# Optimization experiments

Hardware: AMD Instinct MI355X
Metric: run time of the kernel (lower is better)

The kernel has to match this reference:

```python
import jax, jax.numpy as jnp
import numpy as np

ALPHA = 1.0
M = K = N = 4096
VMAX = 16  # keep int32 accumulation far from overflow


def setup_inputs() -> dict:
    key = jax.random.key(0)
    k0, k1, k2 = jax.random.split(key, 3)
    input_tensor = jax.random.randint(k0, (M, N), 0, VMAX, dtype=jnp.int32)
    mat1 = jax.random.randint(k1, (M, K), 0, VMAX, dtype=jnp.int32)
    mat2 = jax.random.randint(k2, (K, N), 0, VMAX, dtype=jnp.int32)
    return {"input_tensor": input_tensor, "mat1": mat1, "mat2": mat2}


def reference(input_tensor, mat1, mat2):
    # int32 GEMM with int32 accumulation (matches torch int32 matmul)
    mm_int32 = jnp.matmul(mat1.astype(jnp.int32), mat2.astype(jnp.int32),
                          preferred_element_type=jnp.int32)
    sum_int32 = mm_int32 + input_tensor  # [M, N] int32
    return sum_int32.astype(jnp.float32) * jnp.float32(ALPHA)
```

## Files before the change

### kernel.cpp

```cpp
#include <hip/hip_runtime.h>

#define MK 4096
#define BK 128

typedef int v4i __attribute__((ext_vector_type(4)));
typedef int v16i __attribute__((ext_vector_type(16)));

#define MFMA32(a, b, c) __builtin_amdgcn_mfma_i32_32x32x32_i8(a, b, c, 0, 0, 0)

#define GLOAD_LDS16(gp, lp) \
  __builtin_amdgcn_global_load_lds((const __attribute__((address_space(1))) void*)(gp), \
                                   (__attribute__((address_space(3))) void*)(lp), 16, 0, 0)

#define SB() __builtin_amdgcn_sched_barrier(0)
#define BARRIER() __builtin_amdgcn_s_barrier()
#define WAIT_VM4() asm volatile("s_waitcnt vmcnt(4)" ::: "memory")
#define WAIT_VM0() asm volatile("s_waitcnt vmcnt(0)" ::: "memory")
#define NOWAIT() ((void)0)

__global__ __launch_bounds__(256) void cvt_kernel(const int* __restrict__ mat1,
                                                  char* __restrict__ A8,
                                                  const int* __restrict__ mat2,
                                                  char* __restrict__ B8T) {
  __shared__ char tile[64][68];
  if (blockIdx.x < 2048) {
    const int n4 = MK * MK / 4;
    int idx = blockIdx.x * 256 + threadIdx.x;
    const int stride = 2048 * 256;
    for (int i = idx; i < n4; i += stride) {
      int4 v = ((const int4*)mat1)[i];
      char4 c;
      c.x = (char)v.x; c.y = (char)v.y; c.z = (char)v.z; c.w = (char)v.w;
      ((char4*)A8)[i] = c;
    }
  } else {
    const int bid = blockIdx.x - 2048;
    const int t = threadIdx.x;
    const int n0 = (bid & 63) * 64, k0 = (bid >> 6) * 64;
#pragma unroll
    for (int r = 0; r < 16; ++r) {
      int k = k0 + r * 4 + (t >> 6);
      int n = n0 + (t & 63);
      tile[t & 63][r * 4 + (t >> 6)] = (char)mat2[(size_t)k * MK + n];
    }
    __syncthreads();
#pragma unroll
    for (int w = 0; w < 4; ++w) {
      int nl = w * 16 + (t >> 4);
      int kl = (t & 15) * 4;
      char4 c = *(const char4*)&tile[nl][kl];
      *(char4*)(B8T + (size_t)(n0 + nl) * MK + k0 + kl) = c;
    }
  }
}

__global__ __launch_bounds__(512, 2) void gemm_i8_kernel(const char* __restrict__ A8,
                                                         const char* __restrict__ B8T,
                                                         const int* __restrict__ inp,
                                                         float* __restrict__ out) {
  extern __shared__ char lds[];
  const int tid = threadIdx.x;
  const int wg = blockIdx.x;
  const int xcd = wg & 7, loc = wg >> 3;
  const int m0 = (((xcd >> 1) << 2) + (loc >> 3)) << 8;
  const int n0 = (((xcd & 1) << 3) + (loc & 7)) << 8;

  const int lane = tid & 63, wid = tid >> 6;
  const int wr = wid >> 2, wc = wid & 3;
  const int rl = lane & 31;
  const int khalf = lane >> 5;

  const int r15 = lane & 15;
  const int slotr = (lane >> 4) ^ ((r15 >> 1) & 3);
  const char* pAr = lds + wr * 8192 + r15 * 64 + slotr * 16;
  const char* pBr = lds + 65536 + wc * 4096 + r15 * 64 + slotr * 16;

  const int sblk = tid >> 7;
  const int skk = (tid >> 6) & 1;
  const int sr15 = (tid >> 2) & 15;
  const int sslot = tid & 3;
  const int sx = sslot ^ ((sr15 >> 1) & 3);
  const int srow = sblk * 32 + (sx & 1) * 16 + sr15;
  const int skb = skk * 32 + (sx >> 1) * 16;
  const char* pA = A8 + (size_t)(m0 + srow) * MK + skb;
  const char* pB = B8T + (size_t)(n0 + srow) * MK + skb;
  char* ldsw = lds + (tid & ~63) * 16;

#define STAGE_A_(NB_, H_, TN_) do {                                               \
    const char* s_ = pA + (TN_)*BK + (H_)*64;                                     \
    GLOAD_LDS16(s_,                    ldsw + ((NB_)*32768 + (H_)*16384));        \
    GLOAD_LDS16(s_ + (size_t)128 * MK, ldsw + ((NB_)*32768 + (H_)*16384 + 8192)); \
  } while (0)
#define STAGE_B_(NB_, H_, TN_) do {                                               \
    const char* s_ = pB + (TN_)*BK + (H_)*64;                                     \
    GLOAD_LDS16(s_,                    ldsw + (65536 + (NB_)*32768 + (H_)*16384)); \
    GLOAD_LDS16(s_ + (size_t)128 * MK, ldsw + (65536 + (NB_)*32768 + (H_)*16384 + 8192)); \
  } while (0)

#define AOFF(B_, KK_, MB_) ((B_)*32768 + ((KK_) >> 1) * 16384 + (MB_)*2048 + ((KK_)&1) * 1024)
#define BOFF(B_, KK_, NB_) ((B_)*32768 + ((KK_) >> 1) * 16384 + (NB_)*2048 + ((KK_)&1) * 1024)

#define REGION(B_, H_, TN_, DOST_, VMW_, DOSYNC_) do {                            \
    bf0 = *(const v4i*)(pBr + BOFF(B_, 2*(H_), 0));                               \
    af0 = *(const v4i*)(pAr + AOFF(B_, 2*(H_), 0));                               \
    af1 = *(const v4i*)(pAr + AOFF(B_, 2*(H_), 1));                               \
    af2 = *(const v4i*)(pAr + AOFF(B_, 2*(H_), 2));                               \
    af3 = *(const v4i*)(pAr + AOFF(B_, 2*(H_), 3));                               \
    bf1 = *(const v4i*)(pBr + BOFF(B_, 2*(H_), 1));                               \
    bg0 = *(const v4i*)(pBr + BOFF(B_, 2*(H_) + 1, 0));                           \
    ag0 = *(const v4i*)(pAr + AOFF(B_, 2*(H_) + 1, 0));                           \
    ag1 = *(const v4i*)(pAr + AOFF(B_, 2*(H_) + 1, 1));                           \
    ag2 = *(const v4i*)(pAr + AOFF(B_, 2*(H_) + 1, 2));                           \
    ag3 = *(const v4i*)(pAr + AOFF(B_, 2*(H_) + 1, 3));                           \
    bg1 = *(const v4i*)(pBr + BOFF(B_, 2*(H_) + 1, 1));                           \
    if (DOST_) STAGE_A_((B_) ^ 1, H_, TN_);                                       \
    __builtin_amdgcn_s_setprio(1);                                                \
    acc[0][0] = MFMA32(af0, bf0, acc[0][0]); acc[1][0] = MFMA32(af1, bf0, acc[1][0]); \
    acc[2][0] = MFMA32(af2, bf0, acc[2][0]); acc[3][0] = MFMA32(af3, bf0, acc[3][0]); \
    acc[0][1] = MFMA32(af0, bf1, acc[0][1]); acc[1][1] = MFMA32(af1, bf1, acc[1][1]); \
    acc[2][1] = MFMA32(af2, bf1, acc[2][1]); acc[3][1] = MFMA32(af3, bf1, acc[3][1]); \
    __builtin_amdgcn_s_setprio(0);                                                \
    if (DOST_) STAGE_B_((B_) ^ 1, H_, TN_);                                       \
    __builtin_amdgcn_s_setprio(1);                                                \
    acc[0][0] = MFMA32(ag0, bg0, acc[0][0]); acc[1][0] = MFMA32(ag1, bg0, acc[1][0]); \
    acc[2][0] = MFMA32(ag2, bg0, acc[2][0]); acc[3][0] = MFMA32(ag3, bg0, acc[3][0]); \
    acc[0][1] = MFMA32(ag0, bg1, acc[0][1]); acc[1][1] = MFMA32(ag1, bg1, acc[1][1]); \
    acc[2][1] = MFMA32(ag2, bg1, acc[2][1]); acc[3][1] = MFMA32(ag3, bg1, acc[3][1]); \
    __builtin_amdgcn_s_setprio(0);                                                \
    if (DOSYNC_) { SB(); VMW_; BARRIER(); SB(); }                                 \
  } while (0)

  v16i acc[4][2];
#pragma unroll
  for (int m = 0; m < 4; ++m)
#pragma unroll
    for (int n = 0; n < 2; ++n)
#pragma unroll
      for (int i = 0; i < 16; ++i) acc[m][n][i] = 0;
  v4i af0, af1, af2, af3, bf0, bf1;
  v4i ag0, ag1, ag2, ag3, bg0, bg1;

  STAGE_A_(0, 0, 0); STAGE_B_(0, 0, 0); STAGE_A_(0, 1, 0); STAGE_B_(0, 1, 0);
  WAIT_VM4(); BARRIER(); SB();

#pragma unroll 1
  for (int it = 0; it < 15; ++it) {
    REGION(0, 0, 2 * it + 1, 1, WAIT_VM4(), 1);
    REGION(0, 1, 2 * it + 1, 1, WAIT_VM4(), 1);
    REGION(1, 0, 2 * it + 2, 1, WAIT_VM4(), 1);
    REGION(1, 1, 2 * it + 2, 1, WAIT_VM4(), 1);
  }
  REGION(0, 0, 31, 1, WAIT_VM4(), 1);
  REGION(0, 1, 31, 1, WAIT_VM4(), 1);
  REGION(1, 0, 0, 0, WAIT_VM0(), 1);
  REGION(1, 1, 0, 0, NOWAIT(), 0);

#pragma unroll
  for (int mb = 0; mb < 4; ++mb) {
#pragma unroll
    for (int nb = 0; nb < 2; ++nb) {
      const int col = n0 + wc * 64 + nb * 32 + rl;
      const int row0 = m0 + wr * 128 + mb * 32 + 4 * khalf;
#pragma unroll
      for (int r = 0; r < 16; ++r) {
        const int row = row0 + (r & 3) + 8 * (r >> 2);
        const size_t idx = (size_t)row * MK + col;
        const int v = acc[mb][nb][r] + __builtin_nontemporal_load(inp + idx);
        __builtin_nontemporal_store((float)v, out + idx);
      }
    }
  }
}

__global__ void fallback_kernel(const int* __restrict__ mat1, const int* __restrict__ mat2,
                                const int* __restrict__ inp, float* __restrict__ out) {
  __shared__ int As[16][16], Bs[16][17];
  int tx = threadIdx.x, ty = threadIdx.y;
  int row = blockIdx.y * 16 + ty, col = blockIdx.x * 16 + tx;
  int acc = 0;
  for (int kt = 0; kt < MK / 16; ++kt) {
    As[ty][tx] = mat1[(size_t)row * MK + kt * 16 + tx];
    Bs[ty][tx] = mat2[(size_t)(kt * 16 + ty) * MK + col];
    __syncthreads();
#pragma unroll
    for (int k = 0; k < 16; ++k) acc += As[ty][k] * Bs[k][tx];
    __syncthreads();
  }
  size_t idx = (size_t)row * MK + col;
  out[idx] = (float)(acc + inp[idx]);
}

extern "C" void kernel_launch(void* const* d_in, const int* in_sizes, int n_in,
                              void* d_out, int out_size, void* d_ws, size_t ws_size,
                              hipStream_t stream) {
  const int* inp = (const int*)d_in[0];
  const int* mat1 = (const int*)d_in[1];
  const int* mat2 = (const int*)d_in[2];
  float* out = (float*)d_out;

  const size_t need = 2 * (size_t)MK * MK;
  if (ws_size >= need) {
    char* A8 = (char*)d_ws;
    char* B8T = A8 + (size_t)MK * MK;
    cvt_kernel<<<6144, 256, 0, stream>>>(mat1, A8, mat2, B8T);
    (void)hipFuncSetAttribute((const void*)gemm_i8_kernel,
                              hipFuncAttributeMaxDynamicSharedMemorySize, 131072);
    gemm_i8_kernel<<<256, 512, 131072, stream>>>(A8, B8T, inp, out);
  } else {
    dim3 blk(16, 16), grd(MK / 16, MK / 16);
    fallback_kernel<<<grd, blk, 0, stream>>>(mat1, mat2, inp, out);
  }
}
```

Baseline: 105.2 us.

## Shrink GEMM tile to 256x128 with 4 waves and triple-buffered BK=64 pipeline

The int8 GEMM moves from 256x256 tiles with 8 waves and a double-buffered BK=128 LDS pipeline to 256x128 tiles with 4 waves, a 3-stage ring of BK=64 stages, and 512 workgroups. The smaller LDS footprint (72KB) lets two workgroups share a CU, and the deeper prefetch (vmcnt 6) keeps more loads in flight. Part of the second half's LDS fragment loads now sit after the first MFMA batch so they overlap with it. In exchange, B data is reused across a narrower tile, so global/L2 traffic per FLOP goes up, and barriers happen twice as often.

```diff
diff --git a/kernel.cpp b/kernel.cpp
--- a/kernel.cpp
+++ b/kernel.cpp
@@ -1,7 +1,6 @@
 #include <hip/hip_runtime.h>
 
 #define MK 4096
-#define BK 128
 
 typedef int v4i __attribute__((ext_vector_type(4)));
 typedef int v16i __attribute__((ext_vector_type(16)));
@@ -14,7 +13,7 @@
 
 #define SB() __builtin_amdgcn_sched_barrier(0)
 #define BARRIER() __builtin_amdgcn_s_barrier()
-#define WAIT_VM4() asm volatile("s_waitcnt vmcnt(4)" ::: "memory")
+#define WAIT_VM6() asm volatile("s_waitcnt vmcnt(6)" ::: "memory")
 #define WAIT_VM0() asm volatile("s_waitcnt vmcnt(0)" ::: "memory")
 #define NOWAIT() ((void)0)
 
@@ -54,7 +53,7 @@
   }
 }
 
-__global__ __launch_bounds__(512, 2) void gemm_i8_kernel(const char* __restrict__ A8,
+__global__ __launch_bounds__(256, 2) void gemm_i8_kernel(const char* __restrict__ A8,
                                                          const char* __restrict__ B8T,
                                                          const int* __restrict__ inp,
                                                          float* __restrict__ out) {
@@ -62,18 +61,18 @@
   const int tid = threadIdx.x;
   const int wg = blockIdx.x;
   const int xcd = wg & 7, loc = wg >> 3;
-  const int m0 = (((xcd >> 1) << 2) + (loc >> 3)) << 8;
-  const int n0 = (((xcd & 1) << 3) + (loc & 7)) << 8;
+  const int m0 = (((xcd >> 2) << 3) + (loc >> 3)) << 8;
+  const int n0 = (((xcd & 3) << 3) + (loc & 7)) << 7;
 
   const int lane = tid & 63, wid = tid >> 6;
-  const int wr = wid >> 2, wc = wid & 3;
+  const int wr = wid >> 1, wc = wid & 1;
   const int rl = lane & 31;
   const int khalf = lane >> 5;
 
   const int r15 = lane & 15;
   const int slotr = (lane >> 4) ^ ((r15 >> 1) & 3);
   const char* pAr = lds + wr * 8192 + r15 * 64 + slotr * 16;
-  const char* pBr = lds + 65536 + wc * 4096 + r15 * 64 + slotr * 16;
+  const char* pBr = lds + 49152 + wc * 4096 + r15 * 64 + slotr * 16;
 
   const int sblk = tid >> 7;
   const int skk = (tid >> 6) & 1;
@@ -84,43 +83,46 @@
   const int skb = skk * 32 + (sx >> 1) * 16;
   const char* pA = A8 + (size_t)(m0 + srow) * MK + skb;
   const char* pB = B8T + (size_t)(n0 + srow) * MK + skb;
-  char* ldsw = lds + (tid & ~63) * 16;
-
-#define STAGE_A_(NB_, H_, TN_) do {                                               \
-    const char* s_ = pA + (TN_)*BK + (H_)*64;                                     \
-    GLOAD_LDS16(s_,                    ldsw + ((NB_)*32768 + (H_)*16384));        \
-    GLOAD_LDS16(s_ + (size_t)128 * MK, ldsw + ((NB_)*32768 + (H_)*16384 + 8192)); \
+  char* ldswA = lds + (tid & ~63) * 16;
+  char* ldswB = lds + 49152 + (tid & ~63) * 16;
+
+#define STAGE_P0(SB_, TN_) do {                                                   \
+    const char* sa_ = pA + (TN_)*64;                                              \
+    GLOAD_LDS16(sa_,                   ldswA + ((SB_)*16384));                    \
+    GLOAD_LDS16(sa_ + (size_t)64 * MK, ldswA + ((SB_)*16384 + 4096));             \
+    GLOAD_LDS16(pB + (TN_)*64,         ldswB + ((SB_)*8192));                     \
   } while (0)
-#define STAGE_B_(NB_, H_, TN_) do {                                               \
-    const char* s_ = pB + (TN_)*BK + (H_)*64;                                     \
-    GLOAD_LDS16(s_,                    ldsw + (65536 + (NB_)*32768 + (H_)*16384)); \
-    GLOAD_LDS16(s_ + (size_t)128 * MK, ldsw + (65536 + (NB_)*32768 + (H_)*16384 + 8192)); \
+#define STAGE_P1(SB_, TN_) do {                                                   \
+    const char* sa_ = pA + (TN_)*64;                                              \
+    GLOAD_LDS16(sa_ + (size_t)128 * MK, ldswA + ((SB_)*16384 + 8192));            \
+    GLOAD_LDS16(sa_ + (size_t)192 * MK, ldswA + ((SB_)*16384 + 12288));           \
+    GLOAD_LDS16(pB + (TN_)*64 + (size_t)64 * MK, ldswB + ((SB_)*8192 + 4096));    \
   } while (0)
 
-#define AOFF(B_, KK_, MB_) ((B_)*32768 + ((KK_) >> 1) * 16384 + (MB_)*2048 + ((KK_)&1) * 1024)
-#define BOFF(B_, KK_, NB_) ((B_)*32768 + ((KK_) >> 1) * 16384 + (NB_)*2048 + ((KK_)&1) * 1024)
-
-#define REGION(B_, H_, TN_, DOST_, VMW_, DOSYNC_) do {                            \
-    bf0 = *(const v4i*)(pBr + BOFF(B_, 2*(H_), 0));                               \
-    af0 = *(const v4i*)(pAr + AOFF(B_, 2*(H_), 0));                               \
-    af1 = *(const v4i*)(pAr + AOFF(B_, 2*(H_), 1));                               \
-    af2 = *(const v4i*)(pAr + AOFF(B_, 2*(H_), 2));                               \
-    af3 = *(const v4i*)(pAr + AOFF(B_, 2*(H_), 3));                               \
-    bf1 = *(const v4i*)(pBr + BOFF(B_, 2*(H_), 1));                               \
-    bg0 = *(const v4i*)(pBr + BOFF(B_, 2*(H_) + 1, 0));                           \
-    ag0 = *(const v4i*)(pAr + AOFF(B_, 2*(H_) + 1, 0));                           \
-    ag1 = *(const v4i*)(pAr + AOFF(B_, 2*(H_) + 1, 1));                           \
-    ag2 = *(const v4i*)(pAr + AOFF(B_, 2*(H_) + 1, 2));                           \
-    ag3 = *(const v4i*)(pAr + AOFF(B_, 2*(H_) + 1, 3));                           \
-    bg1 = *(const v4i*)(pBr + BOFF(B_, 2*(H_) + 1, 1));                           \
-    if (DOST_) STAGE_A_((B_) ^ 1, H_, TN_);                                       \
+#define AOFF(S_, KK_, MB_) ((S_)*16384 + (MB_)*2048 + (KK_)*1024)
+#define BOFF(S_, KK_, NB_) ((S_)*8192 + (NB_)*2048 + (KK_)*1024)
+
+#define REGION(RB_, SB_, TN_, DOST_, VMW_, DOSYNC_) do {                          \
+    bf0 = *(const v4i*)(pBr + BOFF(RB_, 0, 0));                                   \
+    af0 = *(const v4i*)(pAr + AOFF(RB_, 0, 0));                                   \
+    af1 = *(const v4i*)(pAr + AOFF(RB_, 0, 1));                                   \
+    af2 = *(const v4i*)(pAr + AOFF(RB_, 0, 2));                                   \
+    af3 = *(const v4i*)(pAr + AOFF(RB_, 0, 3));                                   \
+    bf1 = *(const v4i*)(pBr + BOFF(RB_, 0, 1));                                   \
+    bg0 = *(const v4i*)(pBr + BOFF(RB_, 1, 0));                                   \
+    ag0 = *(const v4i*)(pAr + AOFF(RB_, 1, 0));                                   \
+    if (DOST_) STAGE_P0(SB_, TN_);                                                \
     __builtin_amdgcn_s_setprio(1);                                                \
     acc[0][0] = MFMA32(af0, bf0, acc[0][0]); acc[1][0] = MFMA32(af1, bf0, acc[1][0]); \
     acc[2][0] = MFMA32(af2, bf0, acc[2][0]); acc[3][0] = MFMA32(af3, bf0, acc[3][0]); \
     acc[0][1] = MFMA32(af0, bf1, acc[0][1]); acc[1][1] = MFMA32(af1, bf1, acc[1][1]); \
     acc[2][1] = MFMA32(af2, bf1, acc[2][1]); acc[3][1] = MFMA32(af3, bf1, acc[3][1]); \
     __builtin_amdgcn_s_setprio(0);                                                \
-    if (DOST_) STAGE_B_((B_) ^ 1, H_, TN_);                                       \
+    ag1 = *(const v4i*)(pAr + AOFF(RB_, 1, 1));                                   \
+    ag2 = *(const v4i*)(pAr + AOFF(RB_, 1, 2));                                   \
+    ag3 = *(const v4i*)(pAr + AOFF(RB_, 1, 3));                                   \
+    bg1 = *(const v4i*)(pBr + BOFF(RB_, 1, 1));                                   \
+    if (DOST_) STAGE_P1(SB_, TN_);                                                \
     __builtin_amdgcn_s_setprio(1);                                                \
     acc[0][0] = MFMA32(ag0, bg0, acc[0][0]); acc[1][0] = MFMA32(ag1, bg0, acc[1][0]); \
     acc[2][0] = MFMA32(ag2, bg0, acc[2][0]); acc[3][0] = MFMA32(ag3, bg0, acc[3][0]); \
@@ -140,20 +142,19 @@
   v4i af0, af1, af2, af3, bf0, bf1;
   v4i ag0, ag1, ag2, ag3, bg0, bg1;
 
-  STAGE_A_(0, 0, 0); STAGE_B_(0, 0, 0); STAGE_A_(0, 1, 0); STAGE_B_(0, 1, 0);
-  WAIT_VM4(); BARRIER(); SB();
+  STAGE_P0(0, 0); STAGE_P1(0, 0); STAGE_P0(1, 1); STAGE_P1(1, 1);
+  SB(); WAIT_VM6(); BARRIER(); SB();
 
 #pragma unroll 1
-  for (int it = 0; it < 15; ++it) {
-    REGION(0, 0, 2 * it + 1, 1, WAIT_VM4(), 1);
-    REGION(0, 1, 2 * it + 1, 1, WAIT_VM4(), 1);
-    REGION(1, 0, 2 * it + 2, 1, WAIT_VM4(), 1);
-    REGION(1, 1, 2 * it + 2, 1, WAIT_VM4(), 1);
-  }
-  REGION(0, 0, 31, 1, WAIT_VM4(), 1);
-  REGION(0, 1, 31, 1, WAIT_VM4(), 1);
-  REGION(1, 0, 0, 0, WAIT_VM0(), 1);
-  REGION(1, 1, 0, 0, NOWAIT(), 0);
+  for (int it = 0; it < 20; ++it) {
+    REGION(0, 2, 3 * it + 2, 1, WAIT_VM6(), 1);
+    REGION(1, 0, 3 * it + 3, 1, WAIT_VM6(), 1);
+    REGION(2, 1, 3 * it + 4, 1, WAIT_VM6(), 1);
+  }
+  REGION(0, 2, 62, 1, WAIT_VM6(), 1);
+  REGION(1, 0, 63, 1, WAIT_VM6(), 1);
+  REGION(2, 0, 0, 0, WAIT_VM0(), 1);
+  REGION(0, 0, 0, 0, NOWAIT(), 0);
 
 #pragma unroll
   for (int mb = 0; mb < 4; ++mb) {
@@ -204,8 +205,8 @@
     char* B8T = A8 + (size_t)MK * MK;
     cvt_kernel<<<6144, 256, 0, stream>>>(mat1, A8, mat2, B8T);
     (void)hipFuncSetAttribute((const void*)gemm_i8_kernel,
-                              hipFuncAttributeMaxDynamicSharedMemorySize, 131072);
-    gemm_i8_kernel<<<256, 512, 131072, stream>>>(A8, B8T, inp, out);
+                              hipFuncAttributeMaxDynamicSharedMemorySize, 73728);
+    gemm_i8_kernel<<<512, 256, 73728, stream>>>(A8, B8T, inp, out);
   } else {
     dim3 blk(16, 16), grd(MK / 16, MK / 16);
     fallback_kernel<<<grd, blk, 0, stream>>>(mat1, mat2, inp, out);
```

Result: slower. 113.7 us (+8.1%).

## Prefetch bias input during GEMM main loop and defer second-half LDS fragment loads

Applied to the files above, without the earlier changes.

Spreads the 128 per-thread loads of the int32 bias input across the 64 K-loop regions, two per region, and adds each one into the accumulators one region later, so the epilogue only converts and stores. The goal is to hide the epilogue's global-load latency behind MFMA work. The loop is fully unrolled so register indices are compile-time constants, and the vmcnt waits are raised from 4 to 6 to cover the extra outstanding loads. The four second-half A/B fragment LDS reads are also moved after the first MFMA group, which lowers register pressure but may expose LDS latency. The full unroll increases code size and instruction-cache pressure.

```diff
diff --git a/kernel.cpp b/kernel.cpp
--- a/kernel.cpp
+++ b/kernel.cpp
@@ -15,6 +15,7 @@
 #define SB() __builtin_amdgcn_sched_barrier(0)
 #define BARRIER() __builtin_amdgcn_s_barrier()
 #define WAIT_VM4() asm volatile("s_waitcnt vmcnt(4)" ::: "memory")
+#define WAIT_VM6() asm volatile("s_waitcnt vmcnt(6)" ::: "memory")
 #define WAIT_VM0() asm volatile("s_waitcnt vmcnt(0)" ::: "memory")
 #define NOWAIT() ((void)0)
 
@@ -86,6 +87,10 @@
   const char* pB = B8T + (size_t)(n0 + srow) * MK + skb;
   char* ldsw = lds + (tid & ~63) * 16;
 
+  const int* pI0 = inp + (size_t)(m0 + wr * 128 + 4 * khalf) * MK + (n0 + wc * 64 + rl);
+  const int* pI1 = pI0 + 32;
+#define IOFF(P_) (((((P_) >> 4) * 32) + (((P_) & 15) & 3) + 8 * (((P_) & 15) >> 2)) * MK)
+
 #define STAGE_A_(NB_, H_, TN_) do {                                               \
     const char* s_ = pA + (TN_)*BK + (H_)*64;                                     \
     GLOAD_LDS16(s_,                    ldsw + ((NB_)*32768 + (H_)*16384));        \
@@ -100,7 +105,10 @@
 #define AOFF(B_, KK_, MB_) ((B_)*32768 + ((KK_) >> 1) * 16384 + (MB_)*2048 + ((KK_)&1) * 1024)
 #define BOFF(B_, KK_, NB_) ((B_)*32768 + ((KK_) >> 1) * 16384 + (NB_)*2048 + ((KK_)&1) * 1024)
 
-#define REGION(B_, H_, TN_, DOST_, VMW_, DOSYNC_) do {                            \
+#define REGION(B_, H_, TN_, DOST_, VMW_, DOSYNC_, RIDX_) do {                     \
+    ipv[(RIDX_) & 1][0] = pI0[IOFF(RIDX_)];                                       \
+    ipv[(RIDX_) & 1][1] = pI1[IOFF(RIDX_)];                                       \
+    SB();                                                                         \
     bf0 = *(const v4i*)(pBr + BOFF(B_, 2*(H_), 0));                               \
     af0 = *(const v4i*)(pAr + AOFF(B_, 2*(H_), 0));                               \
     af1 = *(const v4i*)(pAr + AOFF(B_, 2*(H_), 1));                               \
@@ -109,10 +117,6 @@
     bf1 = *(const v4i*)(pBr + BOFF(B_, 2*(H_), 1));                               \
     bg0 = *(const v4i*)(pBr + BOFF(B_, 2*(H_) + 1, 0));                           \
     ag0 = *(const v4i*)(pAr + AOFF(B_, 2*(H_) + 1, 0));                           \
-    ag1 = *(const v4i*)(pAr + AOFF(B_, 2*(H_) + 1, 1));                           \
-    ag2 = *(const v4i*)(pAr + AOFF(B_, 2*(H_) + 1, 2));                           \
-    ag3 = *(const v4i*)(pAr + AOFF(B_, 2*(H_) + 1, 3));                           \
-    bg1 = *(const v4i*)(pBr + BOFF(B_, 2*(H_) + 1, 1));                           \
     if (DOST_) STAGE_A_((B_) ^ 1, H_, TN_);                                       \
     __builtin_amdgcn_s_setprio(1);                                                \
     acc[0][0] = MFMA32(af0, bf0, acc[0][0]); acc[1][0] = MFMA32(af1, bf0, acc[1][0]); \
@@ -120,6 +124,10 @@
     acc[0][1] = MFMA32(af0, bf1, acc[0][1]); acc[1][1] = MFMA32(af1, bf1, acc[1][1]); \
     acc[2][1] = MFMA32(af2, bf1, acc[2][1]); acc[3][1] = MFMA32(af3, bf1, acc[3][1]); \
     __builtin_amdgcn_s_setprio(0);                                                \
+    ag1 = *(const v4i*)(pAr + AOFF(B_, 2*(H_) + 1, 1));                           \
+    ag2 = *(const v4i*)(pAr + AOFF(B_, 2*(H_) + 1, 2));                           \
+    ag3 = *(const v4i*)(pAr + AOFF(B_, 2*(H_) + 1, 3));                           \
+    bg1 = *(const v4i*)(pBr + BOFF(B_, 2*(H_) + 1, 1));                           \
     if (DOST_) STAGE_B_((B_) ^ 1, H_, TN_);                                       \
     __builtin_amdgcn_s_setprio(1);                                                \
     acc[0][0] = MFMA32(ag0, bg0, acc[0][0]); acc[1][0] = MFMA32(ag1, bg0, acc[1][0]); \
@@ -127,8 +135,18 @@
     acc[0][1] = MFMA32(ag0, bg1, acc[0][1]); acc[1][1] = MFMA32(ag1, bg1, acc[1][1]); \
     acc[2][1] = MFMA32(ag2, bg1, acc[2][1]); acc[3][1] = MFMA32(ag3, bg1, acc[3][1]); \
     __builtin_amdgcn_s_setprio(0);                                                \
+    if ((RIDX_) > 0) {                                                            \
+      acc[((RIDX_)-1) >> 4][0][((RIDX_)-1) & 15] += ipv[((RIDX_)-1) & 1][0];      \
+      acc[((RIDX_)-1) >> 4][1][((RIDX_)-1) & 15] += ipv[((RIDX_)-1) & 1][1];      \
+    }                                                                             \
     if (DOSYNC_) { SB(); VMW_; BARRIER(); SB(); }                                 \
   } while (0)
+
+#define QUAD(IT_)                                                                 \
+  REGION(0, 0, 2*(IT_) + 1, 1, WAIT_VM6(), 1, 4*(IT_) + 0);                       \
+  REGION(0, 1, 2*(IT_) + 1, 1, WAIT_VM6(), 1, 4*(IT_) + 1);                       \
+  REGION(1, 0, 2*(IT_) + 2, 1, WAIT_VM6(), 1, 4*(IT_) + 2);                       \
+  REGION(1, 1, 2*(IT_) + 2, 1, WAIT_VM6(), 1, 4*(IT_) + 3);
 
   v16i acc[4][2];
 #pragma unroll
@@ -139,21 +157,21 @@
       for (int i = 0; i < 16; ++i) acc[m][n][i] = 0;
   v4i af0, af1, af2, af3, bf0, bf1;
   v4i ag0, ag1, ag2, ag3, bg0, bg1;
+  int ipv[2][2];
 
   STAGE_A_(0, 0, 0); STAGE_B_(0, 0, 0); STAGE_A_(0, 1, 0); STAGE_B_(0, 1, 0);
   WAIT_VM4(); BARRIER(); SB();
 
-#pragma unroll 1
-  for (int it = 0; it < 15; ++it) {
-    REGION(0, 0, 2 * it + 1, 1, WAIT_VM4(), 1);
-    REGION(0, 1, 2 * it + 1, 1, WAIT_VM4(), 1);
-    REGION(1, 0, 2 * it + 2, 1, WAIT_VM4(), 1);
-    REGION(1, 1, 2 * it + 2, 1, WAIT_VM4(), 1);
-  }
-  REGION(0, 0, 31, 1, WAIT_VM4(), 1);
-  REGION(0, 1, 31, 1, WAIT_VM4(), 1);
-  REGION(1, 0, 0, 0, WAIT_VM0(), 1);
-  REGION(1, 1, 0, 0, NOWAIT(), 0);
+  QUAD(0)  QUAD(1)  QUAD(2)  QUAD(3)  QUAD(4)
+  QUAD(5)  QUAD(6)  QUAD(7)  QUAD(8)  QUAD(9)
+  QUAD(10) QUAD(11) QUAD(12) QUAD(13) QUAD(14)
+  REGION(0, 0, 31, 1, WAIT_VM6(), 1, 60);
+  REGION(0, 1, 31, 1, WAIT_VM6(), 1, 61);
+  REGION(1, 0, 0, 0, WAIT_VM0(), 1, 62);
+  REGION(1, 1, 0, 0, NOWAIT(), 0, 63);
+
+  acc[3][0][15] += ipv[1][0];
+  acc[3][1][15] += ipv[1][1];
 
 #pragma unroll
   for (int mb = 0; mb < 4; ++mb) {
@@ -165,8 +183,7 @@
       for (int r = 0; r < 16; ++r) {
         const int row = row0 + (r & 3) + 8 * (r >> 2);
         const size_t idx = (size_t)row * MK + col;
-        const int v = acc[mb][nb][r] + __builtin_nontemporal_load(inp + idx);
-        __builtin_nontemporal_store((float)v, out + idx);
+        __builtin_nontemporal_store((float)acc[mb][nb][r], out + idx);
       }
     }
   }
```

After: 95.62 us, median of 2. -9.1%, faster.
